# Kernel optimization log

Hardware: AMD Instinct MI355X
Metric: run time of the kernel (lower is better)

Reference implementation:

```python
import jax, jax.numpy as jnp
import numpy as np

DEPTH = 7  # complete binary trees with 2**DEPTH = 128 leaves

B, L = 4096, 128
V, E, OUT = 100000, 128, 3


def setup_inputs() -> dict:
    key = jax.random.key(0)
    ks = jax.random.split(key, 6)
    tokens = jax.random.randint(ks[0], (B, L), 0, V, dtype=jnp.int64)
    embedding = jax.random.normal(ks[1], (V, E), dtype=jnp.float32)
    # tree_layer: Linear(2E -> E); torch stores weight as [out, in]
    W_tree = jax.random.normal(ks[2], (E, 2 * E), dtype=jnp.float32) * (1.0 / np.sqrt(2 * E))
    b_tree = jax.random.normal(ks[3], (E,), dtype=jnp.float32) * 0.01
    # classifier_layer: Linear(E -> OUT)
    W_cls = jax.random.normal(ks[4], (OUT, E), dtype=jnp.float32) * (1.0 / np.sqrt(E))
    b_cls = jax.random.normal(ks[5], (OUT,), dtype=jnp.float32) * 0.01
    return {"tokens": tokens, "embedding": embedding, "W_tree": W_tree,
            "b_tree": b_tree, "W_cls": W_cls, "b_cls": b_cls}


def reference(tokens, embedding, W_tree, b_tree, W_cls, b_cls):
    # Leaf embeddings: gather rows of the embedding table. [B, L, E]
    reps = embedding[tokens]
    # Level-synchronous bottom-up composition (depth-batched across all trees):
    # at each level, pair adjacent nodes, concat features, apply tree_layer + tanh.
    for _ in range(DEPTH):
        left = reps[:, 0::2, :]   # [B, n/2, E]
        right = reps[:, 1::2, :]  # [B, n/2, E]
        combined = jnp.concatenate([left, right], axis=-1)  # [B, n/2, 2E]
        reps = jnp.tanh(jnp.einsum('bnh,eh->bne', combined, W_tree) + b_tree)
    roots = reps[:, 0, :]  # [B, E]
    return roots @ W_cls.T + b_cls  # [B, OUT]
```

## Files before the change

### kernel.cpp

```cpp
#include <hip/hip_runtime.h>
#include <hip/hip_fp16.h>


typedef _Float16 half8 __attribute__((ext_vector_type(8)));
typedef float floatx4 __attribute__((ext_vector_type(4)));

#define STRIDE 264
#define NPAIR 2048

__device__ __forceinline__ float fast_tanh(float x) {
  float e = __expf(2.f * x);
  return 1.f - 2.f * __builtin_amdgcn_rcpf(e + 1.f);
}

__device__ __forceinline__ unsigned pkrtz(float a, float b) {
  auto h = __builtin_amdgcn_cvt_pkrtz(a, b);
  return __builtin_bit_cast(unsigned, h);
}

__device__ __forceinline__ void mfma_k256(const _Float16* arow, const half8 (&Wf)[2][8],
                                          floatx4 (&accO)[2]) {
  floatx4 aA[2], aB[2];
  aA[0] = (floatx4){0.f, 0.f, 0.f, 0.f}; aA[1] = (floatx4){0.f, 0.f, 0.f, 0.f};
  aB[0] = (floatx4){0.f, 0.f, 0.f, 0.f}; aB[1] = (floatx4){0.f, 0.f, 0.f, 0.f};
#pragma unroll
  for (int ks = 0; ks < 4; ++ks) {
    half8 x0 = *(const half8*)(arow + ks * 32);
    half8 x1 = *(const half8*)(arow + (ks + 4) * 32);
    aA[0] = __builtin_amdgcn_mfma_f32_16x16x32_f16(x0, Wf[0][ks],     aA[0], 0, 0, 0);
    aB[0] = __builtin_amdgcn_mfma_f32_16x16x32_f16(x1, Wf[0][ks + 4], aB[0], 0, 0, 0);
    aA[1] = __builtin_amdgcn_mfma_f32_16x16x32_f16(x0, Wf[1][ks],     aA[1], 0, 0, 0);
    aB[1] = __builtin_amdgcn_mfma_f32_16x16x32_f16(x1, Wf[1][ks + 4], aB[1], 0, 0, 0);
  }
  accO[0] = aA[0] + aB[0];
  accO[1] = aA[1] + aB[1];
}

template<int MT, int MOUT>
__device__ __forceinline__ void level_std(
    const _Float16* inb, _Float16* outb,
    const half8 (&Wf)[2][8], const float (&bias)[2],
    int nbase, int l15, int quad)
{
  floatx4 acc[MT][2];
  if (MT == 1) {
    floatx4 a2[2];
    mfma_k256(inb + l15 * STRIDE + quad * 8, Wf, a2);
    acc[0][0] = a2[0]; acc[0][1] = a2[1];
  } else {
#pragma unroll
    for (int m = 0; m < MT; ++m) {
      acc[m][0] = (floatx4){0.f, 0.f, 0.f, 0.f};
      acc[m][1] = (floatx4){0.f, 0.f, 0.f, 0.f};
    }
#pragma unroll
    for (int m = 0; m < MT; ++m) {
      const _Float16* arow = inb + (m * 16 + l15) * STRIDE + quad * 8;
#pragma unroll
      for (int ks = 0; ks < 8; ++ks) {
        half8 a = *(const half8*)(arow + ks * 32);
        acc[m][0] = __builtin_amdgcn_mfma_f32_16x16x32_f16(a, Wf[0][ks], acc[m][0], 0, 0, 0);
        acc[m][1] = __builtin_amdgcn_mfma_f32_16x16x32_f16(a, Wf[1][ks], acc[m][1], 0, 0, 0);
      }
    }
  }

  const int mrow = quad * 4;
#pragma unroll
  for (int m = 0; m < MT; ++m) {
#pragma unroll
    for (int i = 0; i < 2; ++i) {
      const int col = (nbase + i) * 16 + l15;
      const float b = bias[i];
#pragma unroll
      for (int r = 0; r < 4; ++r) {
        const int node = m * 16 + mrow + r;
        if (node < MOUT) {
          float v = fast_tanh(acc[m][i][r] + b);
          outb[(node >> 1) * STRIDE + (node & 1) * 128 + col] = (_Float16)v;
        }
      }
    }
  }
}

__global__ __launch_bounds__(256, 3)
void tree_kernel(const int* __restrict__ tokens,
                 const float* __restrict__ embedding,
                 const float* __restrict__ W_tree,
                 const float* __restrict__ b_tree,
                 const float* __restrict__ W_cls,
                 const float* __restrict__ b_cls,
                 float* __restrict__ out)
{
  __shared__ __align__(16) _Float16 bufA[64 * STRIDE];
  __shared__ __align__(16) _Float16 bufB[32 * STRIDE];
  __shared__ __align__(16) _Float16 bufC[4 * STRIDE];
  __shared__ float wavepart[4][2][3];

  const int tid  = threadIdx.x;
  const int wid  = tid >> 6;
  const int lane = tid & 63;
  const int l15  = lane & 15;
  const int quad = lane >> 4;
  const int nbase = wid * 2;

  half8 Wf[2][8];
#pragma unroll
  for (int i = 0; i < 2; ++i) {
    const int e = (nbase + i) * 16 + l15;
#pragma unroll
    for (int ks = 0; ks < 8; ++ks) {
      const int k = ks * 32 + quad * 8;
      const float4* p = (const float4*)(W_tree + e * 256 + k);
      float4 lo = p[0], hi = p[1];
      half8 f;
      f[0] = (_Float16)lo.x; f[1] = (_Float16)lo.y; f[2] = (_Float16)lo.z; f[3] = (_Float16)lo.w;
      f[4] = (_Float16)hi.x; f[5] = (_Float16)hi.y; f[6] = (_Float16)hi.z; f[7] = (_Float16)hi.w;
      Wf[i][ks] = f;
    }
  }
  float bias[2];
#pragma unroll
  for (int i = 0; i < 2; ++i) bias[i] = b_tree[(nbase + i) * 16 + l15];

  float wc[2][3];
#pragma unroll
  for (int i = 0; i < 2; ++i) {
    const int col = (nbase + i) * 16 + l15;
#pragma unroll
    for (int o = 0; o < 3; ++o) wc[i][o] = W_cls[o * 128 + col];
  }

  const int leaf = tid >> 1;
  const int hh   = tid & 1;

#pragma unroll 1
  for (int p = blockIdx.x; p < NPAIR; p += gridDim.x) {

#pragma unroll 1
    for (int j = 0; j < 2; ++j) {
      const int s = 2 * p + j;
      {
        const int tok = tokens[s * 128 + leaf];
        const float4* src = (const float4*)(embedding + (size_t)tok * 128 + hh * 64);
        uint4* dst = (uint4*)bufA + (leaf >> 1) * 33 + (leaf & 1) * 16 + hh * 8;
#pragma unroll
        for (int jj = 0; jj < 8; ++jj) {
          float4 x = src[2 * jj], y = src[2 * jj + 1];
          uint4 w;
          w.x = pkrtz(x.x, x.y); w.y = pkrtz(x.z, x.w);
          w.z = pkrtz(y.x, y.y); w.w = pkrtz(y.z, y.w);
          dst[jj] = w;
        }
      }
      __syncthreads();
      level_std<4, 64>(bufA, bufB, Wf, bias, nbase, l15, quad);
      __syncthreads();
      level_std<2, 32>(bufB, bufA, Wf, bias, nbase, l15, quad);
      __syncthreads();
      level_std<1, 16>(bufA, bufB, Wf, bias, nbase, l15, quad);
      __syncthreads();
      level_std<1,  8>(bufB, bufA, Wf, bias, nbase, l15, quad);
      __syncthreads();
      level_std<1,  4>(bufA, bufC + j * 2 * STRIDE,
                       Wf, bias, nbase, l15, quad);
      __syncthreads();
    }

    {
      const int rclamp = l15 < 4 ? l15 : 3;
      floatx4 acc[2];
      mfma_k256(bufC + rclamp * STRIDE + quad * 8, Wf, acc);
      const int mrow = quad * 4;
#pragma unroll
      for (int i = 0; i < 2; ++i) {
        const int col = (nbase + i) * 16 + l15;
#pragma unroll
        for (int r = 0; r < 4; ++r) {
          const int mr = mrow + r;
          if (mr < 4) {
            float v = fast_tanh(acc[i][r] + bias[i]);
            bufA[(mr >> 1) * STRIDE + (mr & 1) * 128 + col] = (_Float16)v;
          }
        }
      }
    }
    __syncthreads();

    {
      floatx4 acc[2];
      mfma_k256(bufA + l15 * STRIDE + quad * 8, Wf, acc);
      float part[2][3] = {{0.f, 0.f, 0.f}, {0.f, 0.f, 0.f}};
      if (quad == 0) {
#pragma unroll
        for (int i = 0; i < 2; ++i) {
#pragma unroll
          for (int rr = 0; rr < 2; ++rr) {
            float v = fast_tanh(acc[i][rr] + bias[i]);
#pragma unroll
            for (int o = 0; o < 3; ++o) part[rr][o] = fmaf(v, wc[i][o], part[rr][o]);
          }
        }
      }
#pragma unroll
      for (int rr = 0; rr < 2; ++rr) {
#pragma unroll
        for (int o = 0; o < 3; ++o) {
          float v = part[rr][o];
          v += __shfl_down(v, 8);
          v += __shfl_down(v, 4);
          v += __shfl_down(v, 2);
          v += __shfl_down(v, 1);
          if (lane == 0) wavepart[wid][rr][o] = v;
        }
      }
    }
    __syncthreads();
    if (tid < 6) {
      const int rr = tid / 3, o = tid - 3 * rr;
      float v = wavepart[0][rr][o] + wavepart[1][rr][o]
              + wavepart[2][rr][o] + wavepart[3][rr][o];
      out[(2 * p + rr) * 3 + o] = v + b_cls[o];
    }
  }
}

extern "C" void kernel_launch(void* const* d_in, const int* in_sizes, int n_in,
                              void* d_out, int out_size, void* d_ws, size_t ws_size,
                              hipStream_t stream) {
  const int*   tokens    = (const int*)d_in[0];
  const float* embedding = (const float*)d_in[1];
  const float* W_tree    = (const float*)d_in[2];
  const float* b_tree    = (const float*)d_in[3];
  const float* W_cls     = (const float*)d_in[4];
  const float* b_cls     = (const float*)d_in[5];
  float* out = (float*)d_out;

  dim3 grid(768), block(256);
  tree_kernel<<<grid, block, 0, stream>>>(tokens, embedding, W_tree, b_tree, W_cls, b_cls, out);
}
```

Before: 156.8 us.

## Compute tree levels in place in one LDS buffer to raise occupancy

Drops the second ping-pong LDS buffer. Each level now reads and writes a single shared buffer at row offsets, with an extra barrier before the first level writes over its own input. Two trees each keep 8 nodes in bufC, so both trees share the level-4 and level-3 steps. With less LDS per block, launch bounds go to 4 blocks per CU and the grid to 1024 blocks, in exchange for holding more values in registers before the write and one more barrier.

```diff
diff --git a/kernel.cpp b/kernel.cpp
--- a/kernel.cpp
+++ b/kernel.cpp
@@ -36,17 +36,16 @@
   accO[1] = aA[1] + aB[1];
 }
 
-template<int MT, int MOUT>
-__device__ __forceinline__ void level_std(
+template<int MT, int MOUT, int INROW, int OUTROW, bool SPLIT, bool CLAMP8>
+__device__ __forceinline__ void level_ip(
     const _Float16* inb, _Float16* outb,
     const half8 (&Wf)[2][8], const float (&bias)[2],
     int nbase, int l15, int quad)
 {
   floatx4 acc[MT][2];
   if (MT == 1) {
-    floatx4 a2[2];
-    mfma_k256(inb + l15 * STRIDE + quad * 8, Wf, a2);
-    acc[0][0] = a2[0]; acc[0][1] = a2[1];
+    const int rr = CLAMP8 ? (l15 < 8 ? l15 : 7) : l15;
+    mfma_k256(inb + (INROW + rr) * STRIDE + quad * 8, Wf, acc[0]);
   } else {
 #pragma unroll
     for (int m = 0; m < MT; ++m) {
@@ -55,7 +54,7 @@
     }
 #pragma unroll
     for (int m = 0; m < MT; ++m) {
-      const _Float16* arow = inb + (m * 16 + l15) * STRIDE + quad * 8;
+      const _Float16* arow = inb + (INROW + m * 16 + l15) * STRIDE + quad * 8;
 #pragma unroll
       for (int ks = 0; ks < 8; ++ks) {
         half8 a = *(const half8*)(arow + ks * 32);
@@ -65,26 +64,35 @@
     }
   }
 
+  _Float16 hv[MT][2][4];
   const int mrow = quad * 4;
 #pragma unroll
-  for (int m = 0; m < MT; ++m) {
+  for (int m = 0; m < MT; ++m)
+#pragma unroll
+    for (int i = 0; i < 2; ++i)
+#pragma unroll
+      for (int r = 0; r < 4; ++r) {
+        const int node = m * 16 + mrow + r;
+        if (node < MOUT) hv[m][i][r] = (_Float16)fast_tanh(acc[m][i][r] + bias[i]);
+      }
+
+  if (SPLIT) __syncthreads();
+
+#pragma unroll
+  for (int m = 0; m < MT; ++m)
 #pragma unroll
     for (int i = 0; i < 2; ++i) {
       const int col = (nbase + i) * 16 + l15;
-      const float b = bias[i];
 #pragma unroll
       for (int r = 0; r < 4; ++r) {
         const int node = m * 16 + mrow + r;
-        if (node < MOUT) {
-          float v = fast_tanh(acc[m][i][r] + b);
-          outb[(node >> 1) * STRIDE + (node & 1) * 128 + col] = (_Float16)v;
-        }
-      }
-    }
-  }
-}
-
-__global__ __launch_bounds__(256, 3)
+        if (node < MOUT)
+          outb[(OUTROW + (node >> 1)) * STRIDE + (node & 1) * 128 + col] = hv[m][i][r];
+      }
+    }
+}
+
+__global__ __launch_bounds__(256, 4)
 void tree_kernel(const int* __restrict__ tokens,
                  const float* __restrict__ embedding,
                  const float* __restrict__ W_tree,
@@ -94,8 +102,7 @@
                  float* __restrict__ out)
 {
   __shared__ __align__(16) _Float16 bufA[64 * STRIDE];
-  __shared__ __align__(16) _Float16 bufB[32 * STRIDE];
-  __shared__ __align__(16) _Float16 bufC[4 * STRIDE];
+  __shared__ __align__(16) _Float16 bufC[8 * STRIDE];
   __shared__ float wavepart[4][2][3];
 
   const int tid  = threadIdx.x;
@@ -155,42 +162,24 @@
         }
       }
       __syncthreads();
-      level_std<4, 64>(bufA, bufB, Wf, bias, nbase, l15, quad);
-      __syncthreads();
-      level_std<2, 32>(bufB, bufA, Wf, bias, nbase, l15, quad);
-      __syncthreads();
-      level_std<1, 16>(bufA, bufB, Wf, bias, nbase, l15, quad);
-      __syncthreads();
-      level_std<1,  8>(bufB, bufA, Wf, bias, nbase, l15, quad);
-      __syncthreads();
-      level_std<1,  4>(bufA, bufC + j * 2 * STRIDE,
-                       Wf, bias, nbase, l15, quad);
-      __syncthreads();
-    }
-
-    {
-      const int rclamp = l15 < 4 ? l15 : 3;
-      floatx4 acc[2];
-      mfma_k256(bufC + rclamp * STRIDE + quad * 8, Wf, acc);
-      const int mrow = quad * 4;
-#pragma unroll
-      for (int i = 0; i < 2; ++i) {
-        const int col = (nbase + i) * 16 + l15;
-#pragma unroll
-        for (int r = 0; r < 4; ++r) {
-          const int mr = mrow + r;
-          if (mr < 4) {
-            float v = fast_tanh(acc[i][r] + bias[i]);
-            bufA[(mr >> 1) * STRIDE + (mr & 1) * 128 + col] = (_Float16)v;
-          }
-        }
-      }
-    }
+      level_ip<4, 64, 0,  0, true,  false>(bufA, bufA, Wf, bias, nbase, l15, quad);
+      __syncthreads();
+      level_ip<2, 32, 0, 32, false, false>(bufA, bufA, Wf, bias, nbase, l15, quad);
+      __syncthreads();
+      level_ip<1, 16, 32, 0, false, false>(bufA, bufA, Wf, bias, nbase, l15, quad);
+      __syncthreads();
+      level_ip<1,  8, 0,  0, false, false>(bufA, bufC + j * 4 * STRIDE, Wf, bias, nbase, l15, quad);
+      __syncthreads();
+    }
+
+    level_ip<1, 8, 0, 0, false, true>(bufC, bufA, Wf, bias, nbase, l15, quad);
+    __syncthreads();
+    level_ip<1, 4, 0, 4, false, false>(bufA, bufA, Wf, bias, nbase, l15, quad);
     __syncthreads();
 
     {
       floatx4 acc[2];
-      mfma_k256(bufA + l15 * STRIDE + quad * 8, Wf, acc);
+      mfma_k256(bufA + (4 + l15) * STRIDE + quad * 8, Wf, acc);
       float part[2][3] = {{0.f, 0.f, 0.f}, {0.f, 0.f, 0.f}};
       if (quad == 0) {
 #pragma unroll
@@ -237,6 +226,6 @@
   const float* b_cls     = (const float*)d_in[5];
   float* out = (float*)d_out;
 
-  dim3 grid(768), block(256);
+  dim3 grid(1024), block(256);
   tree_kernel<<<grid, block, 0, stream>>>(tokens, embedding, W_tree, b_tree, W_cls, b_cls, out);
 }
```

Result: slower. 160.2 us (+2.2%).

## Prefetch next pair's leaf embeddings during root and classifier stages

Applied to the files above, without the earlier changes.

Unrolls the two-tree inner loop and moves the embedding gather for the next tree pair into the tail stages (root combine and classifier), which have little MFMA work. The final levels now write to bufB so bufA is free to receive the prefetch. The gather also uses a new thread-to-row mapping, and launch bounds drop from 3 to 2 blocks per CU, giving more registers at the cost of occupancy. The goal is to hide global-memory gather latency behind compute. The risk is that lower occupancy reduces the latency hiding that came from having other blocks resident.

```diff
diff --git a/kernel.cpp b/kernel.cpp
--- a/kernel.cpp
+++ b/kernel.cpp
@@ -6,7 +6,8 @@
 typedef float floatx4 __attribute__((ext_vector_type(4)));
 
 #define STRIDE 264
-#define NPAIR 2048
+#define UROW   33
+#define NPAIR  2048
 
 __device__ __forceinline__ float fast_tanh(float x) {
   float e = __expf(2.f * x);
@@ -16,6 +17,21 @@
 __device__ __forceinline__ unsigned pkrtz(float a, float b) {
   auto h = __builtin_amdgcn_cvt_pkrtz(a, b);
   return __builtin_bit_cast(unsigned, h);
+}
+
+template<int J0, int J1>
+__device__ __forceinline__ void gather_chunk(int tok, const float* __restrict__ emb,
+                                             _Float16* buf, int row, int seg) {
+  const float4* src = (const float4*)emb + (size_t)tok * 32 + (seg & 1) * 16;
+  uint4* dst = (uint4*)buf + row * UROW + seg * 8;
+#pragma unroll
+  for (int j = J0; j < J1; ++j) {
+    float4 x = src[2 * j], y = src[2 * j + 1];
+    uint4 w;
+    w.x = pkrtz(x.x, x.y); w.y = pkrtz(x.z, x.w);
+    w.z = pkrtz(y.x, y.y); w.w = pkrtz(y.z, y.w);
+    dst[j] = w;
+  }
 }
 
 __device__ __forceinline__ void mfma_k256(const _Float16* arow, const half8 (&Wf)[2][8],
@@ -67,24 +83,22 @@
 
   const int mrow = quad * 4;
 #pragma unroll
-  for (int m = 0; m < MT; ++m) {
+  for (int m = 0; m < MT; ++m)
 #pragma unroll
     for (int i = 0; i < 2; ++i) {
       const int col = (nbase + i) * 16 + l15;
-      const float b = bias[i];
 #pragma unroll
       for (int r = 0; r < 4; ++r) {
         const int node = m * 16 + mrow + r;
         if (node < MOUT) {
-          float v = fast_tanh(acc[m][i][r] + b);
+          float v = fast_tanh(acc[m][i][r] + bias[i]);
           outb[(node >> 1) * STRIDE + (node & 1) * 128 + col] = (_Float16)v;
         }
       }
     }
-  }
-}
-
-__global__ __launch_bounds__(256, 3)
+}
+
+__global__ __launch_bounds__(256, 2)
 void tree_kernel(const int* __restrict__ tokens,
                  const float* __restrict__ embedding,
                  const float* __restrict__ W_tree,
@@ -104,6 +118,8 @@
   const int l15  = lane & 15;
   const int quad = lane >> 4;
   const int nbase = wid * 2;
+  const int row  = tid & 63;
+  const int seg  = tid >> 6;
 
   half8 Wf[2][8];
 #pragma unroll
@@ -132,43 +148,49 @@
     for (int o = 0; o < 3; ++o) wc[i][o] = W_cls[o * 128 + col];
   }
 
-  const int leaf = tid >> 1;
-  const int hh   = tid & 1;
+  {
+    const int tok = tokens[(2 * blockIdx.x) * 128 + 2 * row + (seg >> 1)];
+    gather_chunk<0, 8>(tok, embedding, bufA, row, seg);
+  }
+  __syncthreads();
 
 #pragma unroll 1
   for (int p = blockIdx.x; p < NPAIR; p += gridDim.x) {
-
-#pragma unroll 1
-    for (int j = 0; j < 2; ++j) {
-      const int s = 2 * p + j;
-      {
-        const int tok = tokens[s * 128 + leaf];
-        const float4* src = (const float4*)(embedding + (size_t)tok * 128 + hh * 64);
-        uint4* dst = (uint4*)bufA + (leaf >> 1) * 33 + (leaf & 1) * 16 + hh * 8;
-#pragma unroll
-        for (int jj = 0; jj < 8; ++jj) {
-          float4 x = src[2 * jj], y = src[2 * jj + 1];
-          uint4 w;
-          w.x = pkrtz(x.x, x.y); w.y = pkrtz(x.z, x.w);
-          w.z = pkrtz(y.x, y.y); w.w = pkrtz(y.z, y.w);
-          dst[jj] = w;
-        }
-      }
-      __syncthreads();
-      level_std<4, 64>(bufA, bufB, Wf, bias, nbase, l15, quad);
-      __syncthreads();
-      level_std<2, 32>(bufB, bufA, Wf, bias, nbase, l15, quad);
-      __syncthreads();
-      level_std<1, 16>(bufA, bufB, Wf, bias, nbase, l15, quad);
-      __syncthreads();
-      level_std<1,  8>(bufB, bufA, Wf, bias, nbase, l15, quad);
-      __syncthreads();
-      level_std<1,  4>(bufA, bufC + j * 2 * STRIDE,
-                       Wf, bias, nbase, l15, quad);
-      __syncthreads();
-    }
+    int pn = p + gridDim.x;
+    if (pn >= NPAIR) pn = p;
+    int tokn;
+
+    level_std<4, 64>(bufA, bufB, Wf, bias, nbase, l15, quad);
+    __syncthreads();
+    level_std<2, 32>(bufB, bufA, Wf, bias, nbase, l15, quad);
+    __syncthreads();
+    level_std<1, 16>(bufA, bufB, Wf, bias, nbase, l15, quad);
+    __syncthreads();
+    level_std<1,  8>(bufB, bufA, Wf, bias, nbase, l15, quad);
+    __syncthreads();
+    level_std<1,  4>(bufA, bufC,            Wf, bias, nbase, l15, quad);
+    __syncthreads();
 
     {
+      const int tok = tokens[(2 * p + 1) * 128 + 2 * row + (seg >> 1)];
+      gather_chunk<0, 8>(tok, embedding, bufA, row, seg);
+      tokn = tokens[(2 * pn) * 128 + 2 * row + (seg >> 1)];
+    }
+    __syncthreads();
+
+    level_std<4, 64>(bufA, bufB, Wf, bias, nbase, l15, quad);
+    __syncthreads();
+    level_std<2, 32>(bufB, bufA, Wf, bias, nbase, l15, quad);
+    __syncthreads();
+    level_std<1, 16>(bufA, bufB, Wf, bias, nbase, l15, quad);
+    __syncthreads();
+    level_std<1,  8>(bufB, bufA, Wf, bias, nbase, l15, quad);
+    __syncthreads();
+    level_std<1,  4>(bufA, bufC + 2 * STRIDE, Wf, bias, nbase, l15, quad);
+    __syncthreads();
+
+    {
+      gather_chunk<0, 4>(tokn, embedding, bufA, row, seg);
       const int rclamp = l15 < 4 ? l15 : 3;
       floatx4 acc[2];
       mfma_k256(bufC + rclamp * STRIDE + quad * 8, Wf, acc);
@@ -181,7 +203,7 @@
           const int mr = mrow + r;
           if (mr < 4) {
             float v = fast_tanh(acc[i][r] + bias[i]);
-            bufA[(mr >> 1) * STRIDE + (mr & 1) * 128 + col] = (_Float16)v;
+            bufB[(mr >> 1) * STRIDE + (mr & 1) * 128 + col] = (_Float16)v;
           }
         }
       }
@@ -189,8 +211,9 @@
     __syncthreads();
 
     {
+      gather_chunk<4, 8>(tokn, embedding, bufA, row, seg);
       floatx4 acc[2];
-      mfma_k256(bufA + l15 * STRIDE + quad * 8, Wf, acc);
+      mfma_k256(bufB + l15 * STRIDE + quad * 8, Wf, acc);
       float part[2][3] = {{0.f, 0.f, 0.f}, {0.f, 0.f, 0.f}};
       if (quad == 0) {
 #pragma unroll
```

Measured after the change: 183.7 us. +17.1%, slower.
